# Performance work log

Hardware: AMD Instinct MI355X
Metric: run time of the kernel (lower is better)

The kernel has to match this reference:

```python
import jax, jax.numpy as jnp
import numpy as np
from jax import lax

MAX_LENGTH = 64
BATCH = 65536


def setup_inputs() -> dict:
    key = jax.random.key(0)
    ks = jax.random.split(key, 14)
    init = lambda k, shape, fan_in: jax.random.uniform(k, shape, jnp.float32, -1.0, 1.0) / np.sqrt(fan_in)
    return {
        "a": jax.random.randint(ks[0], (BATCH, MAX_LENGTH), 0, 10, dtype=jnp.int64) if jax.config.jax_enable_x64 else jax.random.randint(ks[0], (BATCH, MAX_LENGTH), 0, 10, dtype=jnp.int32),
        "b": jax.random.randint(ks[1], (BATCH, MAX_LENGTH), 0, 10, dtype=jnp.int32),
        "Ea": jax.random.normal(ks[2], (10, 8), jnp.float32),
        "Eb": jax.random.normal(ks[3], (10, 8), jnp.float32),
        "W1": init(ks[4], (64, 18), 18), "b1": init(ks[5], (64,), 18),
        "W2": init(ks[6], (32, 64), 64), "b2": init(ks[7], (32,), 64),
        "Wd": init(ks[8], (10, 32), 32), "bd": init(ks[9], (10,), 32),
        "Wc": init(ks[10], (2, 32), 32), "bc": init(ks[11], (2,), 32),
    }


def reference(a, b, Ea, Eb, W1, b1, W2, b2, Wd, bd, Wc, bc):
    # a, b: [B, L] int digits in [0,10)
    B, L = a.shape
    a_emb = Ea[a]  # [B, L, 8]
    b_emb = Eb[b]  # [B, L, 8]

    def step(carry_in, x):
        ae, be = x  # each [B, 8]
        combined = jnp.concatenate([ae, be, carry_in], axis=1)  # [B, 18]
        h = jax.nn.relu(combined @ W1.T + b1)  # [B, 64]
        h = jax.nn.relu(h @ W2.T + b2)         # [B, 32]
        digit_logit = h @ Wd.T + bd            # [B, 10]
        carry_logit = h @ Wc.T + bc            # [B, 2]
        return jax.nn.softmax(carry_logit, axis=1), (digit_logit, carry_logit)

    carry0 = jnp.zeros((B, 2), dtype=a_emb.dtype).at[:, 0].set(1.0)
    xs = (jnp.swapaxes(a_emb, 0, 1), jnp.swapaxes(b_emb, 0, 1))  # [L, B, 8]
    _, (digit_logits, carry_logits) = lax.scan(step, carry0, xs)
    # [L, B, *] -> [B, L, *]
    return jnp.swapaxes(digit_logits, 0, 1), jnp.swapaxes(carry_logits, 0, 1)
```

## Files before the change

kernel.cpp:

```cpp
#include <hip/hip_runtime.h>
#include <hip/hip_bf16.h>
#include <stdint.h>

#define NBATCH 65536
#define LSEQ   64

typedef __attribute__((ext_vector_type(8))) short short8;
typedef __attribute__((ext_vector_type(4))) float f32x4;
typedef __attribute__((ext_vector_type(4))) int   i32x4;

static __device__ __forceinline__ int pk_bf16(float x, float y){
    union { __hip_bfloat162 h; int i; } u;
    u.h = __float22bfloat162_rn(float2{x, y});
    return u.i;
}

__global__ __launch_bounds__(256, 4)
void mlp_mfma_kernel(const int* __restrict__ a, const int* __restrict__ b,
                     const float* __restrict__ Ea, const float* __restrict__ Eb,
                     const float* __restrict__ W1, const float* __restrict__ b1,
                     const float* __restrict__ W2, const float* __restrict__ b2,
                     const float* __restrict__ Wd, const float* __restrict__ bd,
                     const float* __restrict__ Wc, const float* __restrict__ bc,
                     float* __restrict__ out)
{
    __shared__ float Pab[100*68];
    __shared__ unsigned char pkL[64*64];
    __shared__ float scr[4][32*17];

    const int tid = threadIdx.x;
    const int wv  = tid >> 6;
    const int l   = tid & 63;
    const int q   = l >> 4;
    const int n   = l & 15;

    const int sBase = blockIdx.x * 64;

    {
        const i32x4* ap = (const i32x4*)(a + (size_t)sBase * LSEQ);
        const i32x4* bp = (const i32x4*)(b + (size_t)sBase * LSEQ);
        #pragma unroll
        for (int k = 0; k < 4; k++){
            int v = tid + k*256;
            i32x4 av = ap[v], bv = bp[v];
            int ns = v >> 4, s0 = (v & 15) << 2;
            pkL[(s0+0)*64 + ns] = (unsigned char)(av[0]*10 + bv[0]);
            pkL[(s0+1)*64 + ns] = (unsigned char)(av[1]*10 + bv[1]);
            pkL[(s0+2)*64 + ns] = (unsigned char)(av[2]*10 + bv[2]);
            pkL[(s0+3)*64 + ns] = (unsigned char)(av[3]*10 + bv[3]);
        }
    }

    for (int e = tid; e < 6400; e += 256){
        int p = e >> 6, j = e & 63;
        int da = p / 10, db = p - da*10;
        float acc = b1[j] + W1[j*18 + 17];
        #pragma unroll
        for (int k2 = 0; k2 < 8; k2++){
            acc = fmaf(Ea[da*8 + k2], W1[j*18 + k2],     acc);
            acc = fmaf(Eb[db*8 + k2], W1[j*18 + 8 + k2], acc);
        }
        Pab[p*68 + j] = acc;
    }

    float DcR[16];
    #pragma unroll
    for (int kc = 0; kc < 2; kc++)
        #pragma unroll
        for (int jj = 0; jj < 8; jj++){
            int j = kc*32 + q*8 + jj;
            DcR[kc*8+jj] = W1[j*18 + 16] - W1[j*18 + 17];
        }

    short8 w2f[2][2];
    #pragma unroll
    for (int mt = 0; mt < 2; mt++)
        #pragma unroll
        for (int kc = 0; kc < 2; kc++){
            union { short8 f; i32x4 d; } u;
            int m = mt*16 + n;
            #pragma unroll
            for (int jj = 0; jj < 8; jj += 2){
                int k = kc*32 + q*8 + jj;
                u.d[jj>>1] = pk_bf16(W2[m*64 + k], W2[m*64 + k + 1]);
            }
            w2f[mt][kc] = u.f;
        }

    short8 w3f;
    {
        union { short8 f; i32x4 d; } u;
        #pragma unroll
        for (int jj = 0; jj < 8; jj += 2){
            int k = q*8 + jj;
            float x0 = 0.f, x1 = 0.f;
            if (n < 10)      { x0 = Wd[n*32+k];      x1 = Wd[n*32+k+1]; }
            else if (n < 12) { x0 = Wc[(n-10)*32+k]; x1 = Wc[(n-10)*32+k+1]; }
            u.d[jj>>1] = pk_bf16(x0, x1);
        }
        w3f = u.f;
    }

    float b2r[8], b3r[4];
    #pragma unroll
    for (int mt = 0; mt < 2; mt++)
        #pragma unroll
        for (int r = 0; r < 4; r++) b2r[mt*4+r] = b2[mt*16 + q*4 + r];
    #pragma unroll
    for (int r = 0; r < 4; r++){
        int m = q*4 + r;
        b3r[r] = (m < 10) ? bd[m] : (m < 12 ? bc[m-10] : 0.f);
    }

    __syncthreads();

    const int tn = sBase + wv*16 + n;
    float carry = 1.0f;
    float* scrw = scr[wv];
    float2* __restrict__ o2 = (float2*)out;
    const unsigned long long cbase2 = (unsigned long long)NBATCH * LSEQ * 5ull;
    const unsigned long long obase  = (unsigned long long)tn * LSEQ;

    for (int s = 0; s < LSEQ; s++){
        const int idx = pkL[s*64 + wv*16 + n];
        const float* prow = Pab + idx*68 + q*8;

        short8 h1f[2];
        #pragma unroll
        for (int kc = 0; kc < 2; kc++){
            f32x4 p0 = *(const f32x4*)(prow + kc*32);
            f32x4 p1 = *(const f32x4*)(prow + kc*32 + 4);
            float h[8];
            #pragma unroll
            for (int jj = 0; jj < 4; jj++){
                h[jj]   = fmaxf(fmaf(carry, DcR[kc*8+jj],   p0[jj]), 0.f);
                h[jj+4] = fmaxf(fmaf(carry, DcR[kc*8+jj+4], p1[jj]), 0.f);
            }
            union { short8 f; i32x4 d; } u;
            u.d[0] = pk_bf16(h[0], h[1]);
            u.d[1] = pk_bf16(h[2], h[3]);
            u.d[2] = pk_bf16(h[4], h[5]);
            u.d[3] = pk_bf16(h[6], h[7]);
            h1f[kc] = u.f;
        }

        f32x4 acc2a = { b2r[0], b2r[1], b2r[2], b2r[3] };
        f32x4 acc2b = { b2r[4], b2r[5], b2r[6], b2r[7] };
        acc2a = __builtin_amdgcn_mfma_f32_16x16x32_bf16(w2f[0][0], h1f[0], acc2a, 0,0,0);
        acc2a = __builtin_amdgcn_mfma_f32_16x16x32_bf16(w2f[0][1], h1f[1], acc2a, 0,0,0);
        acc2b = __builtin_amdgcn_mfma_f32_16x16x32_bf16(w2f[1][0], h1f[0], acc2b, 0,0,0);
        acc2b = __builtin_amdgcn_mfma_f32_16x16x32_bf16(w2f[1][1], h1f[1], acc2b, 0,0,0);

        #pragma unroll
        for (int r = 0; r < 4; r++){
            scrw[(q*4 + r)*17 + n]      = acc2a[r];
            scrw[(16 + q*4 + r)*17 + n] = acc2b[r];
        }
        __builtin_amdgcn_wave_barrier();
        short8 h2f;
        {
            float h[8];
            #pragma unroll
            for (int jj = 0; jj < 8; jj++)
                h[jj] = fmaxf(scrw[(q*8 + jj)*17 + n], 0.f);
            __builtin_amdgcn_wave_barrier();
            union { short8 f; i32x4 d; } u;
            u.d[0] = pk_bf16(h[0], h[1]);
            u.d[1] = pk_bf16(h[2], h[3]);
            u.d[2] = pk_bf16(h[4], h[5]);
            u.d[3] = pk_bf16(h[6], h[7]);
            h2f = u.f;
        }

        f32x4 acc3 = { b3r[0], b3r[1], b3r[2], b3r[3] };
        acc3 = __builtin_amdgcn_mfma_f32_16x16x32_bf16(w3f, h2f, acc3, 0,0,0);

        float diff = acc3[2] - acc3[3];
        int dv = __builtin_amdgcn_ds_bpermute((32+n) << 2, __float_as_int(diff));
        carry = 1.0f / (1.0f + __expf(-__int_as_float(dv)));

        const unsigned long long ss = obase + (unsigned)s;
        const unsigned long long d2 = ss * 5ull;
        if (q == 0){
            o2[d2+0] = float2{acc3[0], acc3[1]};
            o2[d2+1] = float2{acc3[2], acc3[3]};
        } else if (q == 1){
            o2[d2+2] = float2{acc3[0], acc3[1]};
            o2[d2+3] = float2{acc3[2], acc3[3]};
        } else if (q == 2){
            o2[d2+4] = float2{acc3[0], acc3[1]};
            o2[cbase2 + ss] = float2{acc3[2], acc3[3]};
        }
    }
}

extern "C" void kernel_launch(void* const* d_in, const int* in_sizes, int n_in,
                              void* d_out, int out_size, void* d_ws, size_t ws_size,
                              hipStream_t stream) {
    const int*   a  = (const int*)d_in[0];
    const int*   b  = (const int*)d_in[1];
    const float* Ea = (const float*)d_in[2];
    const float* Eb = (const float*)d_in[3];
    const float* W1 = (const float*)d_in[4];
    const float* b1 = (const float*)d_in[5];
    const float* W2 = (const float*)d_in[6];
    const float* b2 = (const float*)d_in[7];
    const float* Wd = (const float*)d_in[8];
    const float* bd = (const float*)d_in[9];
    const float* Wc = (const float*)d_in[10];
    const float* bc = (const float*)d_in[11];

    mlp_mfma_kernel<<<NBATCH / 64, 256, 0, stream>>>(a, b, Ea, Eb, W1, b1,
                                                     W2, b2, Wd, bd, Wc, bc,
                                                     (float*)d_out);
}
```

Before: 312.8 us.

## Switch recurrent MLP to fp16 MFMA with packed math and prefetched tables

Converts the precomputed layer-1 table and the weights to fp16, and computes the layer-1 carry update and ReLU with packed half8 vector ops. The layer-2 output is packed to fp16 before the LDS transpose, which halves scratch traffic. The next step's table rows are prefetched two steps ahead, and outputs for 8 steps are staged and written as wider stores using 32-bit offsets. This targets ALU, LDS and store overhead on the serial recurrence, at the cost of fp16 range and precision (round-toward-zero conversion) and more registers.

```diff
diff --git a/kernel.cpp b/kernel.cpp
--- a/kernel.cpp
+++ b/kernel.cpp
@@ -5,13 +5,15 @@
 #define NBATCH 65536
 #define LSEQ   64
 
-typedef __attribute__((ext_vector_type(8))) short short8;
+typedef __attribute__((ext_vector_type(8))) _Float16 half8;
+typedef __attribute__((ext_vector_type(2))) __fp16  fp16x2;
 typedef __attribute__((ext_vector_type(4))) float f32x4;
+typedef __attribute__((ext_vector_type(4), aligned(8))) float f32x4u;
 typedef __attribute__((ext_vector_type(4))) int   i32x4;
 
-static __device__ __forceinline__ int pk_bf16(float x, float y){
-    union { __hip_bfloat162 h; int i; } u;
-    u.h = __float22bfloat162_rn(float2{x, y});
+static __device__ __forceinline__ int relu_pk_f16(float x, float y){
+    union { fp16x2 h; int i; } u;
+    u.h = __builtin_amdgcn_cvt_pkrtz(fmaxf(x, 0.f), fmaxf(y, 0.f));
     return u.i;
 }
 
@@ -24,9 +26,9 @@
                      const float* __restrict__ Wc, const float* __restrict__ bc,
                      float* __restrict__ out)
 {
-    __shared__ float Pab[100*68];
+    __shared__ __attribute__((aligned(16))) _Float16 Pab[100*72];
     __shared__ unsigned char pkL[64*64];
-    __shared__ float scr[4][32*17];
+    __shared__ int scr[4][16*17 + 16];
 
     const int tid = threadIdx.x;
     const int wv  = tid >> 6;
@@ -60,136 +62,140 @@
             acc = fmaf(Ea[da*8 + k2], W1[j*18 + k2],     acc);
             acc = fmaf(Eb[db*8 + k2], W1[j*18 + 8 + k2], acc);
         }
-        Pab[p*68 + j] = acc;
-    }
-
-    float DcR[16];
+        Pab[p*72 + j] = (_Float16)acc;
+    }
+
+    half8 dcr[2];
     #pragma unroll
-    for (int kc = 0; kc < 2; kc++)
+    for (int kc = 0; kc < 2; kc++){
+        union { half8 v; _Float16 e[8]; } ud;
         #pragma unroll
         for (int jj = 0; jj < 8; jj++){
             int j = kc*32 + q*8 + jj;
-            DcR[kc*8+jj] = W1[j*18 + 16] - W1[j*18 + 17];
-        }
-
-    short8 w2f[2][2];
+            ud.e[jj] = (_Float16)(W1[j*18 + 16] - W1[j*18 + 17]);
+        }
+        dcr[kc] = ud.v;
+    }
+
+    half8 w2f[2][2];
     #pragma unroll
     for (int mt = 0; mt < 2; mt++)
         #pragma unroll
         for (int kc = 0; kc < 2; kc++){
-            union { short8 f; i32x4 d; } u;
+            union { half8 v; _Float16 e[8]; } uw;
             int m = mt*16 + n;
             #pragma unroll
-            for (int jj = 0; jj < 8; jj += 2){
-                int k = kc*32 + q*8 + jj;
-                u.d[jj>>1] = pk_bf16(W2[m*64 + k], W2[m*64 + k + 1]);
-            }
-            w2f[mt][kc] = u.f;
-        }
-
-    short8 w3f;
+            for (int jj = 0; jj < 8; jj++)
+                uw.e[jj] = (_Float16)W2[m*64 + kc*32 + q*8 + jj];
+            w2f[mt][kc] = uw.v;
+        }
+
+    half8 w3f;
     {
-        union { short8 f; i32x4 d; } u;
-        #pragma unroll
-        for (int jj = 0; jj < 8; jj += 2){
+        union { half8 v; _Float16 e[8]; } u3;
+        #pragma unroll
+        for (int jj = 0; jj < 8; jj++){
             int k = q*8 + jj;
-            float x0 = 0.f, x1 = 0.f;
-            if (n < 10)      { x0 = Wd[n*32+k];      x1 = Wd[n*32+k+1]; }
-            else if (n < 12) { x0 = Wc[(n-10)*32+k]; x1 = Wc[(n-10)*32+k+1]; }
-            u.d[jj>>1] = pk_bf16(x0, x1);
-        }
-        w3f = u.f;
-    }
-
-    float b2r[8], b3r[4];
-    #pragma unroll
-    for (int mt = 0; mt < 2; mt++)
-        #pragma unroll
-        for (int r = 0; r < 4; r++) b2r[mt*4+r] = b2[mt*16 + q*4 + r];
+            float x = 0.f;
+            if (n < 10)      x = Wd[n*32+k];
+            else if (n < 12) x = Wc[(n-10)*32+k];
+            u3.e[jj] = (_Float16)x;
+        }
+        w3f = u3.v;
+    }
+
+    f32x4 bias2a = { b2[q*4+0], b2[q*4+1], b2[q*4+2], b2[q*4+3] };
+    f32x4 bias2b = { b2[16+q*4+0], b2[16+q*4+1], b2[16+q*4+2], b2[16+q*4+3] };
+    f32x4 bias3;
     #pragma unroll
     for (int r = 0; r < 4; r++){
         int m = q*4 + r;
-        b3r[r] = (m < 10) ? bd[m] : (m < 12 ? bc[m-10] : 0.f);
+        bias3[r] = (m < 10) ? bd[m] : (m < 12 ? bc[m-10] : 0.f);
     }
 
     __syncthreads();
 
     const int tn = sBase + wv*16 + n;
+    const int lc = wv*16 + n;
+    int* scrw = scr[wv];
+    char* outc = (char*)out;
+    const unsigned dbase = (unsigned)tn*2560u + (unsigned)q*16u;
+    const unsigned cbase = (unsigned)(NBATCH*(size_t)LSEQ*10*4) + (unsigned)tn*512u;
+    const int bpa = (32 + n) << 2;
+
     float carry = 1.0f;
-    float* scrw = scr[wv];
-    float2* __restrict__ o2 = (float2*)out;
-    const unsigned long long cbase2 = (unsigned long long)NBATCH * LSEQ * 5ull;
-    const unsigned long long obase  = (unsigned long long)tn * LSEQ;
-
-    for (int s = 0; s < LSEQ; s++){
-        const int idx = pkL[s*64 + wv*16 + n];
-        const float* prow = Pab + idx*68 + q*8;
-
-        short8 h1f[2];
-        #pragma unroll
-        for (int kc = 0; kc < 2; kc++){
-            f32x4 p0 = *(const f32x4*)(prow + kc*32);
-            f32x4 p1 = *(const f32x4*)(prow + kc*32 + 4);
-            float h[8];
+    int idxN;
+    half8 PA[2][2];
+    {
+        int i0 = pkL[lc];
+        const _Float16* r0 = &Pab[i0*72 + q*8];
+        PA[0][0] = *(const half8*)r0;
+        PA[0][1] = *(const half8*)(r0 + 32);
+        idxN = pkL[64 + lc];
+    }
+
+    for (int so = 0; so < LSEQ; so += 8){
+        f32x4 stg[8];
+        #pragma unroll
+        for (int u = 0; u < 8; u++){
+            const int s = so + u;
+            const int cur = u & 1, nxt = cur ^ 1;
+
+            _Float16 ch = (_Float16)carry;
+            half8 c8 = {ch,ch,ch,ch,ch,ch,ch,ch};
+            half8 z  = {};
+            half8 h10 = __builtin_elementwise_max(PA[cur][0] + c8*dcr[0], z);
+            half8 h11 = __builtin_elementwise_max(PA[cur][1] + c8*dcr[1], z);
+
+            {
+                const _Float16* rn = &Pab[idxN*72 + q*8];
+                PA[nxt][0] = *(const half8*)rn;
+                PA[nxt][1] = *(const half8*)(rn + 32);
+            }
+            int idxN2 = pkL[(((s+2)&63)<<6) + lc];
+
+            f32x4 acc2a = bias2a, acc2b = bias2b;
+            acc2a = __builtin_amdgcn_mfma_f32_16x16x32_f16(w2f[0][0], h10, acc2a, 0,0,0);
+            acc2a = __builtin_amdgcn_mfma_f32_16x16x32_f16(w2f[0][1], h11, acc2a, 0,0,0);
+            acc2b = __builtin_amdgcn_mfma_f32_16x16x32_f16(w2f[1][0], h10, acc2b, 0,0,0);
+            acc2b = __builtin_amdgcn_mfma_f32_16x16x32_f16(w2f[1][1], h11, acc2b, 0,0,0);
+
+            scrw[(2*q+0)*17 + n]   = relu_pk_f16(acc2a[0], acc2a[1]);
+            scrw[(2*q+1)*17 + n]   = relu_pk_f16(acc2a[2], acc2a[3]);
+            scrw[(8+2*q+0)*17 + n] = relu_pk_f16(acc2b[0], acc2b[1]);
+            scrw[(8+2*q+1)*17 + n] = relu_pk_f16(acc2b[2], acc2b[3]);
+            __builtin_amdgcn_wave_barrier();
+            int d0 = scrw[(q*4+0)*17 + n];
+            int d1 = scrw[(q*4+1)*17 + n];
+            int d2 = scrw[(q*4+2)*17 + n];
+            int d3 = scrw[(q*4+3)*17 + n];
+            __builtin_amdgcn_wave_barrier();
+            union { i32x4 d; half8 v; } uh2;
+            uh2.d = i32x4{d0, d1, d2, d3};
+
+            f32x4 acc3 = bias3;
+            acc3 = __builtin_amdgcn_mfma_f32_16x16x32_f16(w3f, uh2.v, acc3, 0,0,0);
+
+            float diff = acc3[2] - acc3[3];
+            int dv = __builtin_amdgcn_ds_bpermute(bpa, __float_as_int(diff));
+            carry = 1.0f / (1.0f + __expf(-__int_as_float(dv)));
+
+            stg[u] = acc3;
+            idxN = idxN2;
+        }
+
+        const unsigned dbq = dbase + (unsigned)so*40u;
+        const unsigned cbq = cbase + (unsigned)so*8u;
+        if (q < 2){
             #pragma unroll
-            for (int jj = 0; jj < 4; jj++){
-                h[jj]   = fmaxf(fmaf(carry, DcR[kc*8+jj],   p0[jj]), 0.f);
-                h[jj+4] = fmaxf(fmaf(carry, DcR[kc*8+jj+4], p1[jj]), 0.f);
+            for (int u = 0; u < 8; u++)
+                *(f32x4u*)(outc + dbq + u*40) = stg[u];
+        } else if (q == 2){
+            #pragma unroll
+            for (int u = 0; u < 8; u++){
+                *(float2*)(outc + dbq + u*40) = float2{stg[u][0], stg[u][1]};
+                *(float2*)(outc + cbq + u*8)  = float2{stg[u][2], stg[u][3]};
             }
-            union { short8 f; i32x4 d; } u;
-            u.d[0] = pk_bf16(h[0], h[1]);
-            u.d[1] = pk_bf16(h[2], h[3]);
-            u.d[2] = pk_bf16(h[4], h[5]);
-            u.d[3] = pk_bf16(h[6], h[7]);
-            h1f[kc] = u.f;
-        }
-
-        f32x4 acc2a = { b2r[0], b2r[1], b2r[2], b2r[3] };
-        f32x4 acc2b = { b2r[4], b2r[5], b2r[6], b2r[7] };
-        acc2a = __builtin_amdgcn_mfma_f32_16x16x32_bf16(w2f[0][0], h1f[0], acc2a, 0,0,0);
-        acc2a = __builtin_amdgcn_mfma_f32_16x16x32_bf16(w2f[0][1], h1f[1], acc2a, 0,0,0);
-        acc2b = __builtin_amdgcn_mfma_f32_16x16x32_bf16(w2f[1][0], h1f[0], acc2b, 0,0,0);
-        acc2b = __builtin_amdgcn_mfma_f32_16x16x32_bf16(w2f[1][1], h1f[1], acc2b, 0,0,0);
-
-        #pragma unroll
-        for (int r = 0; r < 4; r++){
-            scrw[(q*4 + r)*17 + n]      = acc2a[r];
-            scrw[(16 + q*4 + r)*17 + n] = acc2b[r];
-        }
-        __builtin_amdgcn_wave_barrier();
-        short8 h2f;
-        {
-            float h[8];
-            #pragma unroll
-            for (int jj = 0; jj < 8; jj++)
-                h[jj] = fmaxf(scrw[(q*8 + jj)*17 + n], 0.f);
-            __builtin_amdgcn_wave_barrier();
-            union { short8 f; i32x4 d; } u;
-            u.d[0] = pk_bf16(h[0], h[1]);
-            u.d[1] = pk_bf16(h[2], h[3]);
-            u.d[2] = pk_bf16(h[4], h[5]);
-            u.d[3] = pk_bf16(h[6], h[7]);
-            h2f = u.f;
-        }
-
-        f32x4 acc3 = { b3r[0], b3r[1], b3r[2], b3r[3] };
-        acc3 = __builtin_amdgcn_mfma_f32_16x16x32_bf16(w3f, h2f, acc3, 0,0,0);
-
-        float diff = acc3[2] - acc3[3];
-        int dv = __builtin_amdgcn_ds_bpermute((32+n) << 2, __float_as_int(diff));
-        carry = 1.0f / (1.0f + __expf(-__int_as_float(dv)));
-
-        const unsigned long long ss = obase + (unsigned)s;
-        const unsigned long long d2 = ss * 5ull;
-        if (q == 0){
-            o2[d2+0] = float2{acc3[0], acc3[1]};
-            o2[d2+1] = float2{acc3[2], acc3[3]};
-        } else if (q == 1){
-            o2[d2+2] = float2{acc3[0], acc3[1]};
-            o2[d2+3] = float2{acc3[2], acc3[3]};
-        } else if (q == 2){
-            o2[d2+4] = float2{acc3[0], acc3[1]};
-            o2[cbase2 + ss] = float2{acc3[2], acc3[3]};
         }
     }
 }
```

Result: faster. 288.2 us (-7.9%).
